# Kernel optimization log

Measured on AMD Instinct MI355X. Metric: run time of the kernel, lower is better.

Reference implementation:

```python
import jax, jax.numpy as jnp
import numpy as np

D_MODEL = 1024
NUM_HEADS = 16
D_K = D_MODEL // NUM_HEADS
CLAMP = 1e9
EPS = 1e-12


def setup_inputs() -> dict:
    key = jax.random.key(0)
    ks = jax.random.split(key, 11)
    B, S, D = 4, 2048, D_MODEL
    std = 1.0 / np.sqrt(D)
    inp = {
        'Q': jax.random.normal(ks[0], (B, S, D), jnp.float32),
        'K': jax.random.normal(ks[1], (B, S, D), jnp.float32),
        'V': jax.random.normal(ks[2], (B, S, D), jnp.float32),
        'Wq': jax.random.normal(ks[3], (D, D), jnp.float32) * std,
        'bq': jnp.zeros((D,), jnp.float32),
        'Wk': jax.random.normal(ks[4], (D, D), jnp.float32) * std,
        'bk': jnp.zeros((D,), jnp.float32),
        'Wv': jax.random.normal(ks[5], (D, D), jnp.float32) * std,
        'bv': jnp.zeros((D,), jnp.float32),
        'Wo': jax.random.normal(ks[6], (D, D), jnp.float32) * std,
        'bo': jnp.zeros((D,), jnp.float32),
    }
    return inp


def _split_heads(x):
    b, s, _ = x.shape
    return x.reshape(b, s, NUM_HEADS, D_K).transpose(0, 2, 1, 3)  # [b,h,s,dk]


def reference(Q, K, V, Wq, bq, Wk, bk, Wv, bv, Wo, bo):
    Qh = _split_heads(Q @ Wq.T + bq)
    Kh = _split_heads(K @ Wk.T + bk)
    Vh = _split_heads(V @ Wv.T + bv)
    scale = jnp.sqrt(jnp.asarray(D_K, Qh.dtype))
    scores = jnp.einsum('bhqd,bhkd->bhqk', Qh, Kh) / scale
    scores = scores - jnp.max(scores, axis=-1, keepdims=True)
    scores = jnp.clip(scores, -CLAMP, CLAMP)
    attn = jax.nn.softmax(scores, axis=-1)
    attn = jnp.clip(attn, EPS, None)
    attn = attn / jnp.sum(attn, axis=-1, keepdims=True)
    ctx = jnp.einsum('bhqk,bhkd->bhqd', attn, Vh)
    b, h, s, dk = ctx.shape
    ctx = ctx.transpose(0, 2, 1, 3).reshape(b, s, D_MODEL)
    return ctx @ Wo.T + bo
```

## Files before the change

kernel.cpp:

```cpp
#include <hip/hip_runtime.h>
#include <hip/hip_bf16.h>


typedef float  f32x4  __attribute__((ext_vector_type(4)));
typedef __bf16 bf16x8 __attribute__((ext_vector_type(8)));
typedef short  s16x8  __attribute__((ext_vector_type(8)));
typedef int    i32x4  __attribute__((ext_vector_type(4)));

#define MFMA16(a,b,c) __builtin_amdgcn_mfma_f32_16x16x32_bf16((a),(b),(c),0,0,0)

__device__ __forceinline__ unsigned short f2bf(float f) {
    union { float f; unsigned u; } v; v.f = f;
    unsigned r = v.u + 0x7fffu + ((v.u >> 16) & 1u);
    return (unsigned short)(r >> 16);
}

__device__ __forceinline__ s16x8 cvt8(const float* __restrict__ p) {
    f32x4 x = *(const f32x4*)p;
    f32x4 y = *(const f32x4*)(p + 4);
    s16x8 r;
    r[0] = (short)f2bf(x[0]); r[1] = (short)f2bf(x[1]);
    r[2] = (short)f2bf(x[2]); r[3] = (short)f2bf(x[3]);
    r[4] = (short)f2bf(y[0]); r[5] = (short)f2bf(y[1]);
    r[6] = (short)f2bf(y[2]); r[7] = (short)f2bf(y[3]);
    return r;
}

__device__ __forceinline__ void gl_lds16(const void* g, void* l) {
    __builtin_amdgcn_global_load_lds(
        (const __attribute__((address_space(1))) unsigned int*)g,
        (__attribute__((address_space(3))) unsigned int*)l, 16, 0, 0);
}

__device__ __forceinline__ float exp2_fast(float x) {
    float r;
    asm("v_exp_f32 %0, %1" : "=v"(r) : "v"(x));
    return r;
}

__device__ __forceinline__ int cvtpk_bf16(float lo, float hi) {
    int r;
    asm("v_cvt_pk_bf16_f32 %0, %1, %2" : "=v"(r) : "v"(lo), "v"(hi));
    return r;
}
__device__ __forceinline__ s16x8 pk8(f32x4 x, f32x4 y) {
    i32x4 r;
    r[0] = cvtpk_bf16(x[0], x[1]);
    r[1] = cvtpk_bf16(x[2], x[3]);
    r[2] = cvtpk_bf16(y[0], y[1]);
    r[3] = cvtpk_bf16(y[2], y[3]);
    return __builtin_bit_cast(s16x8, r);
}
__device__ __forceinline__ void plswap32(int& a, int& b) {
    asm("v_permlane32_swap_b32 %0, %1" : "+v"(a), "+v"(b));
}
__device__ __forceinline__ void plswap16(int& a, int& b) {
    asm("v_permlane16_swap_b32 %0, %1" : "+v"(a), "+v"(b));
}

__device__ __forceinline__ void pack_pf(const f32x4 pe[4], bf16x8& pf0, bf16x8& pf1) {
    int a0 = cvtpk_bf16(pe[0][0], pe[0][1]);
    int a1 = cvtpk_bf16(pe[0][2], pe[0][3]);
    int b0 = cvtpk_bf16(pe[1][0], pe[1][1]);
    int b1 = cvtpk_bf16(pe[1][2], pe[1][3]);
    plswap32(a0, b0); plswap32(a1, b1);
    plswap16(a0, b0); plswap16(a1, b1);
    i32x4 f0; f0[0] = a0; f0[1] = a1; f0[2] = b0; f0[3] = b1;
    int c0 = cvtpk_bf16(pe[2][0], pe[2][1]);
    int c1 = cvtpk_bf16(pe[2][2], pe[2][3]);
    int d0 = cvtpk_bf16(pe[3][0], pe[3][1]);
    int d1 = cvtpk_bf16(pe[3][2], pe[3][3]);
    plswap32(c0, d0); plswap32(c1, d1);
    plswap16(c0, d0); plswap16(c1, d1);
    i32x4 f1; f1[0] = c0; f1[1] = c1; f1[2] = d0; f1[3] = d1;
    pf0 = __builtin_bit_cast(bf16x8, f0);
    pf1 = __builtin_bit_cast(bf16x8, f1);
}

__global__ __launch_bounds__(256) void cvt_kernel(
    const float* __restrict__ src, unsigned short* __restrict__ dst, int n8)
{
    int i = blockIdx.x * 256 + threadIdx.x;
    if (i < n8) *(s16x8*)(dst + (size_t)i * 8) = cvt8(src + (size_t)i * 8);
}

__global__ __launch_bounds__(256) void proj_kernel(
    const float* __restrict__ Qf, const float* __restrict__ Kf,
    const float* __restrict__ Vf,
    const float* __restrict__ Wqf, const float* __restrict__ Wkf,
    const float* __restrict__ Wvf,
    const float* __restrict__ bqf, const float* __restrict__ bkf,
    const float* __restrict__ bvf,
    unsigned short* __restrict__ Qh, unsigned short* __restrict__ Kh,
    unsigned short* __restrict__ Vtw, float qscale)
{
    constexpr int K = 1024;
    __shared__ unsigned short Ash[128 * 32];
    __shared__ unsigned short Bsh[128 * 32];

    const int t    = threadIdx.x;
    const int w    = t >> 6;
    const int lane = t & 63;
    const int wm   = w >> 1, wn = w & 1;
    const int lr   = lane & 15, quad = lane >> 4;

    const int z = blockIdx.z;
    const float *Af, *Wf, *bias;
    float scale;
    unsigned short* out;
    if (z == 0)      { Af = Qf;  Wf = Wqf; bias = bqf; out = Qh;  scale = qscale; }
    else if (z == 1) { Af = Kf;  Wf = Wkf; bias = bkf; out = Kh;  scale = 1.0f; }
    else             { Af = Wvf; Wf = Vf;  bias = bvf; out = Vtw; scale = 1.0f; }

    int m0, n0;
    if (z < 2) {
        m0 = (blockIdx.x * 8 + (blockIdx.y >> 3)) * 128;
        n0 = (blockIdx.y & 7) * 128;
    } else {
        m0 = (blockIdx.y & 7) * 128;
        n0 = (blockIdx.x * 8 + (blockIdx.y >> 3)) * 128;
    }

    const int srow = t >> 2;
    const int skp  = (t & 3) * 8;

    const float* Ap0 = Af + (size_t)(m0 + srow) * K + skp;
    const float* Ap1 = Ap0 + (size_t)64 * K;
    const float* Wp0 = Wf + (size_t)(n0 + srow) * K + skp;
    const float* Wp1 = Wp0 + (size_t)64 * K;
    unsigned short* dA = &Ash[srow * 32 + skp];
    unsigned short* dB = &Bsh[srow * 32 + skp];

    f32x4 a0x, a0y, a1x, a1y, w0x, w0y, w1x, w1y;
#define LOADP(kk) do {                                                        \
        a0x = *(const f32x4*)(Ap0 + (kk)); a0y = *(const f32x4*)(Ap0 + (kk) + 4); \
        a1x = *(const f32x4*)(Ap1 + (kk)); a1y = *(const f32x4*)(Ap1 + (kk) + 4); \
        w0x = *(const f32x4*)(Wp0 + (kk)); w0y = *(const f32x4*)(Wp0 + (kk) + 4); \
        w1x = *(const f32x4*)(Wp1 + (kk)); w1y = *(const f32x4*)(Wp1 + (kk) + 4); \
    } while (0)

    f32x4 acc[4][4] = {};
    LOADP(0);

    for (int k0 = 0; k0 < K; k0 += 32) {
        __syncthreads();
        *(s16x8*)dA              = pk8(a0x, a0y);
        *(s16x8*)(dA + 64 * 32)  = pk8(a1x, a1y);
        *(s16x8*)dB              = pk8(w0x, w0y);
        *(s16x8*)(dB + 64 * 32)  = pk8(w1x, w1y);
        const int kn = (k0 + 32) & 1023;
        LOADP(kn);
        __syncthreads();

        bf16x8 af[4], bw[4];
#pragma unroll
        for (int i = 0; i < 4; i++)
            af[i] = *(const bf16x8*)&Ash[(wm * 64 + i * 16 + lr) * 32 + quad * 8];
#pragma unroll
        for (int j = 0; j < 4; j++)
            bw[j] = *(const bf16x8*)&Bsh[(wn * 64 + j * 16 + lr) * 32 + quad * 8];

#pragma unroll
        for (int i = 0; i < 4; i++)
#pragma unroll
            for (int j = 0; j < 4; j++)
                acc[i][j] = MFMA16(af[i], bw[j], acc[i][j]);
    }
#undef LOADP

#pragma unroll
    for (int i = 0; i < 4; i++) {
#pragma unroll
        for (int j = 0; j < 4; j++) {
            const int n = n0 + wn * 64 + j * 16 + lr;
#pragma unroll
            for (int r = 0; r < 4; r++) {
                const int m = m0 + wm * 64 + i * 16 + quad * 4 + r;
                float val = (acc[i][j][r] + ((z == 2) ? bias[m] : bias[n])) * scale;
                if (z < 2) {
                    const int b = m >> 11, s = m & 2047, h = n >> 6, d = n & 63;
                    out[(((size_t)(b * 16 + h) * 2048 + s) << 6) + d] = f2bf(val);
                } else {
                    const int h = m >> 6, d = m & 63, b = n >> 11, s = n & 2047;
                    out[((size_t)(b * 16 + h) * 64 + d) * 2048 + s] = f2bf(val);
                }
            }
        }
    }
}

__global__ __launch_bounds__(256) void gemm_o(
    const unsigned short* __restrict__ A,
    const unsigned short* __restrict__ W,
    const float* __restrict__ bias,
    float* __restrict__ out)
{
    constexpr int K = 1024;
    __shared__ unsigned short Ash[2 * 128 * 32];
    __shared__ unsigned short Bsh[2 * 128 * 32];

    const int t    = threadIdx.x;
    const int w    = t >> 6;
    const int lane = t & 63;
    const int wm   = w >> 1, wn = w & 1;
    const int lr   = lane & 15, quad = lane >> 4;

    const int bid  = blockIdx.y * 8 + blockIdx.x;
    const int orig = (bid & 7) * 64 + (bid >> 3);
    const int n0 = (orig & 7) * 128;
    const int m0 = (orig >> 3) * 128;

    const int srow = t >> 2;
    const int skp  = (t & 3) * 8;

    const unsigned short* Ap0 = A + (size_t)(m0 + srow) * K + skp;
    const unsigned short* Ap1 = Ap0 + (size_t)64 * K;
    const unsigned short* Wp0 = W + (size_t)(n0 + srow) * K + skp;
    const unsigned short* Wp1 = Wp0 + (size_t)64 * K;
    unsigned short* lA0 = &Ash[w * 512];
    unsigned short* lA1 = &Ash[2048 + w * 512];
    unsigned short* lB0 = &Bsh[w * 512];
    unsigned short* lB1 = &Bsh[2048 + w * 512];

#define STAGE(buf, k0) do {                       \
        gl_lds16(Ap0 + (k0), lA0 + (buf) * 4096); \
        gl_lds16(Ap1 + (k0), lA1 + (buf) * 4096); \
        gl_lds16(Wp0 + (k0), lB0 + (buf) * 4096); \
        gl_lds16(Wp1 + (k0), lB1 + (buf) * 4096); \
    } while (0)

    f32x4 acc[4][4] = {};

    STAGE(0, 0);
    int cur = 0;

    for (int k0 = 0; k0 < K; k0 += 32) {
        if (k0 + 32 < K) {
            STAGE(cur ^ 1, k0 + 32);
            asm volatile("s_waitcnt vmcnt(4)" ::: "memory");
        } else {
            asm volatile("s_waitcnt vmcnt(0)" ::: "memory");
        }
        __builtin_amdgcn_s_barrier();
        __builtin_amdgcn_sched_barrier(0);

        bf16x8 af[4], bw[4];
#pragma unroll
        for (int i = 0; i < 4; i++)
            af[i] = *(const bf16x8*)&Ash[cur * 4096 + (wm * 64 + i * 16 + lr) * 32 + quad * 8];
#pragma unroll
        for (int j = 0; j < 4; j++)
            bw[j] = *(const bf16x8*)&Bsh[cur * 4096 + (wn * 64 + j * 16 + lr) * 32 + quad * 8];

#pragma unroll
        for (int i = 0; i < 4; i++)
#pragma unroll
            for (int j = 0; j < 4; j++)
                acc[i][j] = MFMA16(af[i], bw[j], acc[i][j]);

        __builtin_amdgcn_sched_barrier(0);
        __builtin_amdgcn_s_barrier();
        cur ^= 1;
    }
#undef STAGE

#pragma unroll
    for (int i = 0; i < 4; i++) {
#pragma unroll
        for (int j = 0; j < 4; j++) {
            const int n = n0 + wn * 64 + j * 16 + lr;
#pragma unroll
            for (int r = 0; r < 4; r++) {
                const int m = m0 + wm * 64 + i * 16 + quad * 4 + r;
                out[(size_t)m * 1024 + n] = acc[i][j][r] + bias[n];
            }
        }
    }
}

__global__ __launch_bounds__(256) void attn_kernel(
    const unsigned short* __restrict__ Qh,
    const unsigned short* __restrict__ Kh,
    const unsigned short* __restrict__ Vt,
    unsigned short* __restrict__ ctx)
{
    constexpr int KS = 72;
    __shared__ unsigned short Ksh[64 * KS];
    __shared__ unsigned short Vts[64 * KS];

    const int t    = threadIdx.x;
    const int w    = t >> 6;
    const int lane = t & 63;
    const int lr   = lane & 15, quad = lane >> 4;

    const int bh = blockIdx.y, qblk = blockIdx.x;
    const size_t base = (size_t)bh * 2048 * 64;
    const unsigned short* Qp = Qh + base;
    const unsigned short* Kg = Kh + base + (size_t)lane * 64 + w * 16;
    const unsigned short* Vg = Vt + base + (size_t)lane * 2048 + w * 16;

    const int q0 = qblk * 128 + w * 32;
    const unsigned short* qr0 = Qp + (size_t)(q0 + lr) * 64;
    const unsigned short* qr1 = Qp + (size_t)(q0 + 16 + lr) * 64;
    bf16x8 aq0 = *(const bf16x8*)(qr0 + quad * 8);
    bf16x8 aq1 = *(const bf16x8*)(qr0 + 32 + quad * 8);
    bf16x8 aq2 = *(const bf16x8*)(qr1 + quad * 8);
    bf16x8 aq3 = *(const bf16x8*)(qr1 + 32 + quad * 8);

    f32x4 Of0[4] = {}, Of1[4] = {};
    float ls0 = 0.f, ls1 = 0.f;

    s16x8 kv0 = *(const s16x8*)(Kg);
    s16x8 kv1 = *(const s16x8*)(Kg + 8);
    s16x8 vv0 = *(const s16x8*)(Vg);
    s16x8 vv1 = *(const s16x8*)(Vg + 8);

    for (int kb = 0; kb < 2048; kb += 64) {
        __syncthreads();
        *(s16x8*)&Ksh[lane * KS + w * 16]     = kv0;
        *(s16x8*)&Ksh[lane * KS + w * 16 + 8] = kv1;
        *(s16x8*)&Vts[lane * KS + w * 16]     = vv0;
        *(s16x8*)&Vts[lane * KS + w * 16 + 8] = vv1;

        const int kn = (kb + 64) & 2047;
        kv0 = *(const s16x8*)(Kg + (size_t)kn * 64);
        kv1 = *(const s16x8*)(Kg + (size_t)kn * 64 + 8);
        vv0 = *(const s16x8*)(Vg + kn);
        vv1 = *(const s16x8*)(Vg + kn + 8);

        __syncthreads();

        f32x4 pe0[4], pe1[4];
#pragma unroll
        for (int nt = 0; nt < 4; nt++) {
            const unsigned short* kr = &Ksh[(16 * nt + lr) * KS + quad * 8];
            bf16x8 k0 = *(const bf16x8*)kr;
            bf16x8 k1 = *(const bf16x8*)(kr + 32);
            f32x4 c0 = {}, c1 = {};
            c0 = MFMA16(k0, aq0, c0); c0 = MFMA16(k1, aq1, c0);
            c1 = MFMA16(k0, aq2, c1); c1 = MFMA16(k1, aq3, c1);
            f32x4 p0, p1;
#pragma unroll
            for (int r = 0; r < 4; r++) p0[r] = exp2_fast(c0[r]);
#pragma unroll
            for (int r = 0; r < 4; r++) p1[r] = exp2_fast(c1[r]);
            ls0 += (p0[0] + p0[1]) + (p0[2] + p0[3]);
            ls1 += (p1[0] + p1[1]) + (p1[2] + p1[3]);
            pe0[nt] = p0; pe1[nt] = p1;
        }

        bf16x8 pf00, pf01, pf10, pf11;
        pack_pf(pe0, pf00, pf01);
        pack_pf(pe1, pf10, pf11);

#pragma unroll
        for (int dt = 0; dt < 4; dt++) {
            const unsigned short* vr = &Vts[(dt * 16 + lr) * KS + quad * 8];
            bf16x8 v0 = *(const bf16x8*)vr;
            bf16x8 v1 = *(const bf16x8*)(vr + 32);
            Of0[dt] = MFMA16(pf00, v0, Of0[dt]);
            Of0[dt] = MFMA16(pf01, v1, Of0[dt]);
            Of1[dt] = MFMA16(pf10, v0, Of1[dt]);
            Of1[dt] = MFMA16(pf11, v1, Of1[dt]);
        }
    }

    ls0 += __shfl_xor(ls0, 16);
    ls0 += __shfl_xor(ls0, 32);
    ls1 += __shfl_xor(ls1, 16);
    ls1 += __shfl_xor(ls1, 32);

    const int b = bh >> 4, h = bh & 15;
#pragma unroll
    for (int r = 0; r < 4; r++) {
        const float inv0 = 1.0f / __shfl(ls0, quad * 4 + r, 64);
        const int qa = q0 + quad * 4 + r;
        unsigned short* cp0 = ctx + ((size_t)b * 2048 + qa) * 1024 + h * 64;
#pragma unroll
        for (int dt = 0; dt < 4; dt++)
            cp0[dt * 16 + lr] = f2bf(Of0[dt][r] * inv0);

        const float inv1 = 1.0f / __shfl(ls1, quad * 4 + r, 64);
        const int qb = q0 + 16 + quad * 4 + r;
        unsigned short* cp1 = ctx + ((size_t)b * 2048 + qb) * 1024 + h * 64;
#pragma unroll
        for (int dt = 0; dt < 4; dt++)
            cp1[dt * 16 + lr] = f2bf(Of1[dt][r] * inv1);
    }
}

extern "C" void kernel_launch(void* const* d_in, const int* in_sizes, int n_in,
                              void* d_out, int out_size, void* d_ws, size_t ws_size,
                              hipStream_t stream) {
    const float* Q  = (const float*)d_in[0];
    const float* K  = (const float*)d_in[1];
    const float* V  = (const float*)d_in[2];
    const float* Wq = (const float*)d_in[3];
    const float* bq = (const float*)d_in[4];
    const float* Wk = (const float*)d_in[5];
    const float* bk = (const float*)d_in[6];
    const float* Wv = (const float*)d_in[7];
    const float* bv = (const float*)d_in[8];
    const float* Wo = (const float*)d_in[9];
    const float* bo = (const float*)d_in[10];

    const size_t EB = (size_t)8192 * 1024;
    const size_t EW = (size_t)1024 * 1024;
    unsigned short* Qh  = (unsigned short*)d_ws;
    unsigned short* Kh  = Qh  + EB;
    unsigned short* Vtw = Kh  + EB;
    unsigned short* Ctx = Vtw + EB;
    unsigned short* Wob = Ctx + EB;

    const float QSCALE = 0.125f * 1.44269504088896340736f;

    dim3 tb(256);
    cvt_kernel<<<(int)(EW / 8 / 256), tb, 0, stream>>>(Wo, Wob, (int)(EW / 8));
    proj_kernel<<<dim3(8, 64, 3), tb, 0, stream>>>(
        Q, K, V, Wq, Wk, Wv, bq, bk, bv, Qh, Kh, Vtw, QSCALE);
    attn_kernel<<<dim3(16, 64), tb, 0, stream>>>(Qh, Kh, Vtw, Ctx);
    gemm_o<<<dim3(8, 64), tb, 0, stream>>>(Ctx, Wob, bo, (float*)d_out);
}
```

Baseline: 377.5 us.

## Pre-convert inputs to bf16 and double-buffer projection GEMM via direct LDS loads

A single fused conversion kernel now turns Q, K, V and all four weight matrices into bf16 up front. The projection GEMM then stages bf16 tiles straight into double-buffered shared memory with global_load_lds and vmcnt waits, replacing the register-staged fp32 load, convert and store. The aim is to halve the GEMM's global read traffic and overlap the next tile's load with the current MFMAs. The cost is an extra full pass that reads fp32 and writes bf16 copies of the large activations, plus more workspace (Ctx reuses the Qb buffer).

```diff
diff --git a/kernel.cpp b/kernel.cpp
--- a/kernel.cpp
+++ b/kernel.cpp
@@ -42,14 +42,6 @@
     int r;
     asm("v_cvt_pk_bf16_f32 %0, %1, %2" : "=v"(r) : "v"(lo), "v"(hi));
     return r;
-}
-__device__ __forceinline__ s16x8 pk8(f32x4 x, f32x4 y) {
-    i32x4 r;
-    r[0] = cvtpk_bf16(x[0], x[1]);
-    r[1] = cvtpk_bf16(x[2], x[3]);
-    r[2] = cvtpk_bf16(y[0], y[1]);
-    r[3] = cvtpk_bf16(y[2], y[3]);
-    return __builtin_bit_cast(s16x8, r);
 }
 __device__ __forceinline__ void plswap32(int& a, int& b) {
     asm("v_permlane32_swap_b32 %0, %1" : "+v"(a), "+v"(b));
@@ -77,26 +69,46 @@
     pf1 = __builtin_bit_cast(bf16x8, f1);
 }
 
-__global__ __launch_bounds__(256) void cvt_kernel(
-    const float* __restrict__ src, unsigned short* __restrict__ dst, int n8)
+__global__ __launch_bounds__(256) void cvt4_kernel(
+    const float* __restrict__ Q,  const float* __restrict__ K,
+    const float* __restrict__ V,
+    const float* __restrict__ Wq, const float* __restrict__ Wk,
+    const float* __restrict__ Wv, const float* __restrict__ Wo,
+    unsigned short* __restrict__ Qb, unsigned short* __restrict__ Kb,
+    unsigned short* __restrict__ Vb,
+    unsigned short* __restrict__ Wqb, unsigned short* __restrict__ Wkb,
+    unsigned short* __restrict__ Wvb, unsigned short* __restrict__ Wob)
 {
-    int i = blockIdx.x * 256 + threadIdx.x;
-    if (i < n8) *(s16x8*)(dst + (size_t)i * 8) = cvt8(src + (size_t)i * 8);
+    const int bid = blockIdx.x;
+    const float* s;
+    unsigned short* d;
+    int idx;
+    if (bid < 4096)       { s = Q; d = Qb; idx = bid; }
+    else if (bid < 8192)  { s = K; d = Kb; idx = bid - 4096; }
+    else if (bid < 12288) { s = V; d = Vb; idx = bid - 8192; }
+    else {
+        const int wb = bid - 12288, ws = wb >> 9;
+        idx = wb & 511;
+        s = (ws == 0) ? Wq : (ws == 1) ? Wk : (ws == 2) ? Wv : Wo;
+        d = (ws == 0) ? Wqb : (ws == 1) ? Wkb : (ws == 2) ? Wvb : Wob;
+    }
+    const size_t i = (size_t)idx * 256 + threadIdx.x;
+    *(s16x8*)(d + i * 8) = cvt8(s + i * 8);
 }
 
 __global__ __launch_bounds__(256) void proj_kernel(
-    const float* __restrict__ Qf, const float* __restrict__ Kf,
-    const float* __restrict__ Vf,
-    const float* __restrict__ Wqf, const float* __restrict__ Wkf,
-    const float* __restrict__ Wvf,
+    const unsigned short* __restrict__ Qb, const unsigned short* __restrict__ Kb,
+    const unsigned short* __restrict__ Vb,
+    const unsigned short* __restrict__ Wqb, const unsigned short* __restrict__ Wkb,
+    const unsigned short* __restrict__ Wvb,
     const float* __restrict__ bqf, const float* __restrict__ bkf,
     const float* __restrict__ bvf,
     unsigned short* __restrict__ Qh, unsigned short* __restrict__ Kh,
     unsigned short* __restrict__ Vtw, float qscale)
 {
     constexpr int K = 1024;
-    __shared__ unsigned short Ash[128 * 32];
-    __shared__ unsigned short Bsh[128 * 32];
+    __shared__ unsigned short Ash[2 * 128 * 32];
+    __shared__ unsigned short Bsh[2 * 128 * 32];
 
     const int t    = threadIdx.x;
     const int w    = t >> 6;
@@ -105,12 +117,13 @@
     const int lr   = lane & 15, quad = lane >> 4;
 
     const int z = blockIdx.z;
-    const float *Af, *Wf, *bias;
+    const unsigned short *A, *W;
+    const float* bias;
     float scale;
     unsigned short* out;
-    if (z == 0)      { Af = Qf;  Wf = Wqf; bias = bqf; out = Qh;  scale = qscale; }
-    else if (z == 1) { Af = Kf;  Wf = Wkf; bias = bkf; out = Kh;  scale = 1.0f; }
-    else             { Af = Wvf; Wf = Vf;  bias = bvf; out = Vtw; scale = 1.0f; }
+    if (z == 0)      { A = Qb;  W = Wqb; bias = bqf; out = Qh;  scale = qscale; }
+    else if (z == 1) { A = Kb;  W = Wkb; bias = bkf; out = Kh;  scale = 1.0f; }
+    else             { A = Wvb; W = Vb;  bias = bvf; out = Vtw; scale = 1.0f; }
 
     int m0, n0;
     if (z < 2) {
@@ -124,49 +137,56 @@
     const int srow = t >> 2;
     const int skp  = (t & 3) * 8;
 
-    const float* Ap0 = Af + (size_t)(m0 + srow) * K + skp;
-    const float* Ap1 = Ap0 + (size_t)64 * K;
-    const float* Wp0 = Wf + (size_t)(n0 + srow) * K + skp;
-    const float* Wp1 = Wp0 + (size_t)64 * K;
-    unsigned short* dA = &Ash[srow * 32 + skp];
-    unsigned short* dB = &Bsh[srow * 32 + skp];
-
-    f32x4 a0x, a0y, a1x, a1y, w0x, w0y, w1x, w1y;
-#define LOADP(kk) do {                                                        \
-        a0x = *(const f32x4*)(Ap0 + (kk)); a0y = *(const f32x4*)(Ap0 + (kk) + 4); \
-        a1x = *(const f32x4*)(Ap1 + (kk)); a1y = *(const f32x4*)(Ap1 + (kk) + 4); \
-        w0x = *(const f32x4*)(Wp0 + (kk)); w0y = *(const f32x4*)(Wp0 + (kk) + 4); \
-        w1x = *(const f32x4*)(Wp1 + (kk)); w1y = *(const f32x4*)(Wp1 + (kk) + 4); \
+    const unsigned short* Ap0 = A + (size_t)(m0 + srow) * K + skp;
+    const unsigned short* Ap1 = Ap0 + (size_t)64 * K;
+    const unsigned short* Wp0 = W + (size_t)(n0 + srow) * K + skp;
+    const unsigned short* Wp1 = Wp0 + (size_t)64 * K;
+    unsigned short* lA0 = &Ash[w * 512];
+    unsigned short* lA1 = &Ash[2048 + w * 512];
+    unsigned short* lB0 = &Bsh[w * 512];
+    unsigned short* lB1 = &Bsh[2048 + w * 512];
+
+#define STAGE(buf, k0) do {                       \
+        gl_lds16(Ap0 + (k0), lA0 + (buf) * 4096); \
+        gl_lds16(Ap1 + (k0), lA1 + (buf) * 4096); \
+        gl_lds16(Wp0 + (k0), lB0 + (buf) * 4096); \
+        gl_lds16(Wp1 + (k0), lB1 + (buf) * 4096); \
     } while (0)
 
     f32x4 acc[4][4] = {};
-    LOADP(0);
+
+    STAGE(0, 0);
+    int cur = 0;
 
     for (int k0 = 0; k0 < K; k0 += 32) {
-        __syncthreads();
-        *(s16x8*)dA              = pk8(a0x, a0y);
-        *(s16x8*)(dA + 64 * 32)  = pk8(a1x, a1y);
-        *(s16x8*)dB              = pk8(w0x, w0y);
-        *(s16x8*)(dB + 64 * 32)  = pk8(w1x, w1y);
-        const int kn = (k0 + 32) & 1023;
-        LOADP(kn);
-        __syncthreads();
+        if (k0 + 32 < K) {
+            STAGE(cur ^ 1, k0 + 32);
+            asm volatile("s_waitcnt vmcnt(4)" ::: "memory");
+        } else {
+            asm volatile("s_waitcnt vmcnt(0)" ::: "memory");
+        }
+        __builtin_amdgcn_s_barrier();
+        __builtin_amdgcn_sched_barrier(0);
 
         bf16x8 af[4], bw[4];
 #pragma unroll
         for (int i = 0; i < 4; i++)
-            af[i] = *(const bf16x8*)&Ash[(wm * 64 + i * 16 + lr) * 32 + quad * 8];
+            af[i] = *(const bf16x8*)&Ash[cur * 4096 + (wm * 64 + i * 16 + lr) * 32 + quad * 8];
 #pragma unroll
         for (int j = 0; j < 4; j++)
-            bw[j] = *(const bf16x8*)&Bsh[(wn * 64 + j * 16 + lr) * 32 + quad * 8];
+            bw[j] = *(const bf16x8*)&Bsh[cur * 4096 + (wn * 64 + j * 16 + lr) * 32 + quad * 8];
 
 #pragma unroll
         for (int i = 0; i < 4; i++)
 #pragma unroll
             for (int j = 0; j < 4; j++)
                 acc[i][j] = MFMA16(af[i], bw[j], acc[i][j]);
-    }
-#undef LOADP
+
+        __builtin_amdgcn_sched_barrier(0);
+        __builtin_amdgcn_s_barrier();
+        cur ^= 1;
+    }
+#undef STAGE
 
 #pragma unroll
     for (int i = 0; i < 4; i++) {
@@ -406,18 +426,25 @@
 
     const size_t EB = (size_t)8192 * 1024;
     const size_t EW = (size_t)1024 * 1024;
-    unsigned short* Qh  = (unsigned short*)d_ws;
+    unsigned short* Qb  = (unsigned short*)d_ws;
+    unsigned short* Kb  = Qb  + EB;
+    unsigned short* Vb  = Kb  + EB;
+    unsigned short* Wqb = Vb  + EB;
+    unsigned short* Wkb = Wqb + EW;
+    unsigned short* Wvb = Wkb + EW;
+    unsigned short* Wob = Wvb + EW;
+    unsigned short* Qh  = Wob + EW;
     unsigned short* Kh  = Qh  + EB;
     unsigned short* Vtw = Kh  + EB;
-    unsigned short* Ctx = Vtw + EB;
-    unsigned short* Wob = Ctx + EB;
+    unsigned short* Ctx = Qb;
 
     const float QSCALE = 0.125f * 1.44269504088896340736f;
 
     dim3 tb(256);
-    cvt_kernel<<<(int)(EW / 8 / 256), tb, 0, stream>>>(Wo, Wob, (int)(EW / 8));
+    cvt4_kernel<<<14336, tb, 0, stream>>>(Q, K, V, Wq, Wk, Wv, Wo,
+                                          Qb, Kb, Vb, Wqb, Wkb, Wvb, Wob);
     proj_kernel<<<dim3(8, 64, 3), tb, 0, stream>>>(
-        Q, K, V, Wq, Wk, Wv, bq, bk, bv, Qh, Kh, Vtw, QSCALE);
+        Qb, Kb, Vb, Wqb, Wkb, Wvb, bq, bk, bv, Qh, Kh, Vtw, QSCALE);
     attn_kernel<<<dim3(16, 64), tb, 0, stream>>>(Qh, Kh, Vtw, Ctx);
     gemm_o<<<dim3(8, 64), tb, 0, stream>>>(Ctx, Wob, bo, (float*)d_out);
 }
```

New measurement: 349.3 us. 7.5% less time.
